# Kernel tuning notes

Hardware: AMD Instinct MI355X
Metric: run time of the kernel (lower is better)

## Reference

```python
import jax, jax.numpy as jnp
import numpy as np

U, I, D = 2048, 4096, 64


def setup_inputs() -> dict:
    key = jax.random.key(0)
    ks = jax.random.split(key, 16)
    s = 0.02  # weight scale (xavier-ish)
    inp = {
        "ui_input_mp": jax.random.uniform(ks[0], (U, I), jnp.float32),
        "ui_input_pmp": jax.random.uniform(ks[1], (U, I), jnp.float32),
        "Wu_mp": jax.random.normal(ks[2], (D, I), jnp.float32) * s,
        "Wu_pmp": jax.random.normal(ks[3], (D, I), jnp.float32) * s,
        "Wi_mp": jax.random.normal(ks[4], (D, U), jnp.float32) * s,
        "Wi_pmp": jax.random.normal(ks[5], (D, U), jnp.float32) * s,
        "mw_mp": jax.random.normal(ks[6], (I, D), jnp.float32) * s,
        "mb_mp": jnp.zeros((I,), jnp.float32),
        "aw_mp": jax.random.normal(ks[7], (I, I), jnp.float32) * s,
        "ab_mp": jnp.zeros((I,), jnp.float32),
        "Wat_mp": jax.random.normal(ks[8], (U, U + I), jnp.float32) * s,
        "mw_pmp": jax.random.normal(ks[9], (I, D), jnp.float32) * s,
        "mb_pmp": jnp.zeros((I,), jnp.float32),
        "aw_pmp": jax.random.normal(ks[10], (I, I), jnp.float32) * s,
        "ab_pmp": jnp.zeros((I,), jnp.float32),
        "Wat_pmp": jax.random.normal(ks[11], (U, U + I), jnp.float32) * s,
        "mlp_w": jax.random.normal(ks[12], (D, 2 * D), jnp.float32) * s,
        "mlp_b": jnp.zeros((D,), jnp.float32),
        "tr_w": jax.random.normal(ks[13], (D, D), jnp.float32) * s,
        "tr_b": jnp.zeros((D,), jnp.float32),
    }
    return inp


def _attention_weights(x, mw, mb, aw, ab, Wat):
    # x: [U+I, D]; mlp Linear(D,I)+ReLU (dropout=0), then tanh
    h = jnp.tanh(jax.nn.relu(x @ mw.T + mb))          # [U+I, I]
    a = jnp.tanh(h @ aw.T + ab)                        # [U+I, I]
    scores = Wat @ a                                   # [U, I]
    return jax.nn.softmax(scores, axis=1)


def _branch(ui, Wu, Wi, mw, mb, aw, ab, Wat):
    ue = ui @ Wu.T                                     # [U, D] user embeds
    ie = ui.T @ Wi.T                                   # [I, D] item embeds
    x = jnp.concatenate([ue, ie], axis=0)              # [U+I, D]
    at = _attention_weights(x, mw, mb, aw, ab, Wat)    # [U, I]
    ue_at = at @ ie                                    # [U, D]
    return ue, ie, ue_at


def reference(ui_input_mp, ui_input_pmp, Wu_mp, Wu_pmp, Wi_mp, Wi_pmp,
              mw_mp, mb_mp, aw_mp, ab_mp, Wat_mp,
              mw_pmp, mb_pmp, aw_pmp, ab_pmp, Wat_pmp,
              mlp_w, mlp_b, tr_w, tr_b):
    mlp = lambda z: jax.nn.sigmoid(z @ mlp_w.T + mlp_b)

    ue_mp, ie_mp, ue_mp_at = _branch(ui_input_mp, Wu_mp, Wi_mp,
                                     mw_mp, mb_mp, aw_mp, ab_mp, Wat_mp)
    ue_pmp, ie_pmp, ue_pmp_at = _branch(ui_input_pmp, Wu_pmp, Wi_pmp,
                                        mw_pmp, mb_pmp, aw_pmp, ab_pmp, Wat_pmp)

    u_mp = mlp(jnp.concatenate([ue_mp, ue_mp_at], axis=1))      # [U, D]
    u_pmp = mlp(jnp.concatenate([ue_pmp, ue_pmp_at], axis=1))   # [U, D]

    rate = jax.nn.sigmoid(u_mp + u_pmp)
    user_fusion = rate * u_mp + (1.0 - rate) * u_pmp            # [U, D]

    item_embeddings = mlp(jnp.concatenate([ie_mp, ie_pmp], axis=1))  # [I, D]

    user_embeds = jnp.tanh(user_fusion @ tr_w.T + tr_b)          # [U, D]
    return user_embeds, item_embeddings
```

## Files before the change

kernel.cpp:

```cpp
#include <hip/hip_runtime.h>
#include <stdint.h>
#include <math.h>


typedef short short8 __attribute__((ext_vector_type(8)));
typedef unsigned short ushort8 __attribute__((ext_vector_type(8)));
typedef unsigned char uchar8 __attribute__((ext_vector_type(8)));
typedef float f32x4 __attribute__((ext_vector_type(4)));
typedef int int4v __attribute__((ext_vector_type(4)));
typedef int int8v __attribute__((ext_vector_type(8)));

#define DEVI static __device__ __forceinline__

DEVI unsigned short f2bf(float f) {
  uint32_t u = __builtin_bit_cast(uint32_t, f);
  return (unsigned short)((u + 0x7fffu + ((u >> 16) & 1u)) >> 16);
}
DEVI unsigned char f2fp8(float f) {
  uint32_t u = __builtin_bit_cast(uint32_t, f);
  uint32_t s = (u >> 24) & 0x80u;
  uint32_t a = u & 0x7fffffffu;
  if (a >= 0x43e00000u) return (unsigned char)(s | 0x7eu);
  if (a < 0x3c800000u) {
    float af = __builtin_bit_cast(float, a);
    uint32_t n = (uint32_t)__builtin_rintf(af * 512.0f);
    return (unsigned char)(s | n);
  }
  uint32_t r = a + 0xfffffu + ((a >> 20) & 1u);
  return (unsigned char)(s | ((r >> 20) - 960u));
}
DEVI float sigmoidf_(float x) { return 1.0f / (1.0f + expf(-x)); }

DEVI void gld16(const void* g, void* l) {
  __builtin_amdgcn_global_load_lds(
      (const __attribute__((address_space(1))) unsigned int*)g,
      (__attribute__((address_space(3))) unsigned int*)l, 16, 0, 0);
}

#define MFMA16B(a, b, c) __builtin_amdgcn_mfma_f32_16x16x32_bf16(a, b, c, 0, 0, 0)
#define MFMAMX(a, b, c)                                              \
  __builtin_amdgcn_mfma_scale_f32_16x16x128_f8f6f4(                  \
      a, b, c, 0, 0, 0, 0x7f7f7f7fu, 0, 0x7f7f7f7fu)

__global__ __launch_bounds__(256) void k_f32_to_bf16(
    const float* __restrict__ s, unsigned short* __restrict__ d, long n) {
  long i0 = ((long)blockIdx.x * 256 + threadIdx.x) * 8;
  long stride = (long)gridDim.x * 256 * 8;
  for (long i = i0; i < n; i += stride) {
    f32x4 a = *(const f32x4*)(s + i);
    f32x4 b = *(const f32x4*)(s + i + 4);
    ushort8 o;
    o[0] = f2bf(a[0]); o[1] = f2bf(a[1]); o[2] = f2bf(a[2]); o[3] = f2bf(a[3]);
    o[4] = f2bf(b[0]); o[5] = f2bf(b[1]); o[6] = f2bf(b[2]); o[7] = f2bf(b[3]);
    *(ushort8*)(d + i) = o;
  }
}

__global__ __launch_bounds__(256) void k_f32_to_fp8(
    const float* __restrict__ s, unsigned char* __restrict__ d, long n,
    float scale) {
  long i0 = ((long)blockIdx.x * 256 + threadIdx.x) * 8;
  long stride = (long)gridDim.x * 256 * 8;
  for (long i = i0; i < n; i += stride) {
    f32x4 a = *(const f32x4*)(s + i);
    f32x4 b = *(const f32x4*)(s + i + 4);
    uchar8 o;
    o[0] = f2fp8(a[0] * scale); o[1] = f2fp8(a[1] * scale);
    o[2] = f2fp8(a[2] * scale); o[3] = f2fp8(a[3] * scale);
    o[4] = f2fp8(b[0] * scale); o[5] = f2fp8(b[1] * scale);
    o[6] = f2fp8(b[2] * scale); o[7] = f2fp8(b[3] * scale);
    *(uchar8*)(d + i) = o;
  }
}

template <int EPI>
__global__ __launch_bounds__(256) void k_gemmMX(
    const unsigned char* __restrict__ A0, const unsigned char* __restrict__ A1,
    const unsigned char* __restrict__ B0, const unsigned char* __restrict__ B1,
    float* __restrict__ outF, unsigned char* __restrict__ oB0,
    unsigned char* __restrict__ oB1, const float* __restrict__ bias0,
    const float* __restrict__ bias1, int M, int N, int K, long zsf,
    float dsc) {
  const int gx = gridDim.x;
  const int nwg = gx * gridDim.y;
  const int flat = blockIdx.y * gx + blockIdx.x;
  const int swz = (flat & 7) * (nwg >> 3) + (flat >> 3);
  const int bxi = swz % gx, byi = swz / gx;

  const int bz = blockIdx.z;
  const unsigned char* A = bz ? A1 : A0;
  const unsigned char* B = bz ? B1 : B0;
  unsigned char* outB = bz ? oB1 : oB0;
  const float* bias = bz ? bias1 : bias0;

  __shared__ unsigned char lds[2][2][16384];
  const int tid = threadIdx.x, lane = tid & 63;
  const int wid = tid >> 6, wr = wid >> 1, wc = wid & 1;
  const int bm = bxi * 128, bn = byi * 128;
  const int rl = lane & 15, q = lane >> 4;

  const int x7 = rl & 7;
  const int c0 = ((2 * q) ^ x7) << 4;
  const int c1 = ((2 * q + 1) ^ x7) << 4;

  size_t soff[4];
  int dsto[4];
#pragma unroll
  for (int i = 0; i < 4; i++) {
    const int cid = tid + 256 * i;
    const int r = cid >> 3, c = cid & 7;
    soff[i] = (size_t)r * K + ((c ^ (r & 7)) << 4);
    dsto[i] = cid << 4;
  }

  const unsigned char* gA = A + (size_t)bm * K;
  const unsigned char* gB = B + (size_t)bn * K;

  auto stage = [&](int k0, int buf) {
#pragma unroll
    for (int i = 0; i < 4; i++) {
      gld16(gA + k0 + soff[i], &lds[buf][0][dsto[i]]);
      gld16(gB + k0 + soff[i], &lds[buf][1][dsto[i]]);
    }
  };

  f32x4 acc[4][4] = {};

  stage(0, 0);
  asm volatile("s_waitcnt vmcnt(0)\ns_barrier" ::: "memory");

  int buf = 0;
  for (int k0 = 0; k0 < K; k0 += 128) {
    if (k0 + 128 < K) stage(k0 + 128, buf ^ 1);

    const unsigned char* As = &lds[buf][0][0];
    const unsigned char* Bs = &lds[buf][1][0];
    int8v af[4], bf[4];
#pragma unroll
    for (int mi = 0; mi < 4; mi++) {
      const unsigned char* p = As + (wr * 64 + mi * 16 + rl) * 128;
      int4v lo = *(const int4v*)(p + c0);
      int4v hi = *(const int4v*)(p + c1);
      af[mi] = __builtin_shufflevector(lo, hi, 0, 1, 2, 3, 4, 5, 6, 7);
    }
#pragma unroll
    for (int ni = 0; ni < 4; ni++) {
      const unsigned char* p = Bs + (wc * 64 + ni * 16 + rl) * 128;
      int4v lo = *(const int4v*)(p + c0);
      int4v hi = *(const int4v*)(p + c1);
      bf[ni] = __builtin_shufflevector(lo, hi, 0, 1, 2, 3, 4, 5, 6, 7);
    }

    __builtin_amdgcn_s_setprio(1);
#pragma unroll
    for (int mi = 0; mi < 4; mi++)
#pragma unroll
      for (int ni = 0; ni < 4; ni++)
        acc[mi][ni] = MFMAMX(af[mi], bf[ni], acc[mi][ni]);
    __builtin_amdgcn_s_setprio(0);

    if (k0 + 128 < K) {
      asm volatile("s_waitcnt vmcnt(0)\ns_barrier" ::: "memory");
      buf ^= 1;
    }
  }

#pragma unroll
  for (int mi = 0; mi < 4; mi++) {
#pragma unroll
    for (int ni = 0; ni < 4; ni++) {
      const int col = bn + wc * 64 + ni * 16 + rl;
#pragma unroll
      for (int r = 0; r < 4; r++) {
        const int row = bm + wr * 64 + mi * 16 + q * 4 + r;
        const float v = acc[mi][ni][r] * dsc;
        if (EPI == 0)
          outF[(long)bz * zsf + (size_t)row * N + col] = v;
        else
          outB[(size_t)row * N + col] = f2fp8(tanhf(v + bias[row]));
      }
    }
  }
}

__global__ __launch_bounds__(256) void k_gemmH(
    const unsigned short* __restrict__ A0, const unsigned short* __restrict__ A1,
    const unsigned short* __restrict__ B0, const unsigned short* __restrict__ B1,
    unsigned char* __restrict__ o0, unsigned char* __restrict__ o1,
    const float* __restrict__ bias0, const float* __restrict__ bias1, int M,
    int N, int K) {
  const int bz = blockIdx.z;
  const unsigned short* A = bz ? A1 : A0;
  const unsigned short* B = bz ? B1 : B0;
  unsigned char* out8 = bz ? o1 : o0;
  const float* bias = bz ? bias1 : bias0;

  __shared__ unsigned short As[128 * 32];
  __shared__ unsigned short Bs[128 * 32];
  const int tid = threadIdx.x, lane = tid & 63, wid = tid >> 6;
  const int wr = wid >> 1, wc = wid & 1;
  const int bm = blockIdx.x * 128, bn = blockIdx.y * 128;
  const int c0 = tid, c1 = tid + 256;
  const int s0 = ((c0 & 3) ^ ((c0 >> 3) & 3)) << 3;
  const int s1 = ((c1 & 3) ^ ((c1 >> 3) & 3)) << 3;
  const int rl = lane & 15, q = lane >> 4;
  const int qe = (q ^ ((rl >> 1) & 3)) << 3;

  f32x4 acc[4][4] = {};

  for (int k0 = 0; k0 < K; k0 += 32) {
    gld16(A + (size_t)(bm + (c0 >> 2)) * K + k0 + s0, As + c0 * 8);
    gld16(A + (size_t)(bm + (c1 >> 2)) * K + k0 + s1, As + c1 * 8);
    gld16(B + (size_t)(bn + (c0 >> 2)) * K + k0 + s0, Bs + c0 * 8);
    gld16(B + (size_t)(bn + (c1 >> 2)) * K + k0 + s1, Bs + c1 * 8);
    __syncthreads();

    short8 af[4], bfr[4];
#pragma unroll
    for (int mi = 0; mi < 4; mi++)
      af[mi] = *(const short8*)(As + (wr * 64 + mi * 16 + rl) * 32 + qe);
#pragma unroll
    for (int ni = 0; ni < 4; ni++)
      bfr[ni] = *(const short8*)(Bs + (wc * 64 + ni * 16 + rl) * 32 + qe);
#pragma unroll
    for (int mi = 0; mi < 4; mi++)
#pragma unroll
      for (int ni = 0; ni < 4; ni++)
        acc[mi][ni] = MFMA16B(af[mi], bfr[ni], acc[mi][ni]);
    __syncthreads();
  }

#pragma unroll
  for (int mi = 0; mi < 4; mi++) {
#pragma unroll
    for (int ni = 0; ni < 4; ni++) {
      const int col = bn + wc * 64 + ni * 16 + rl;
#pragma unroll
      for (int r = 0; r < 4; r++) {
        const int row = bm + wr * 64 + mi * 16 + q * 4 + r;
        out8[(size_t)row * N + col] =
            f2fp8(tanhf(fmaxf(acc[mi][ni][r] + bias[col], 0.0f)));
      }
    }
  }
}

template <int AMODE, int BMODE>
__global__ __launch_bounds__(256) void k_sgemm64s(
    const void* __restrict__ A0, const void* __restrict__ A1,
    const void* __restrict__ B0, const void* __restrict__ B1,
    float* __restrict__ P, int kchunk, int lda, int ldb, int M) {
  const int br = blockIdx.z, kz = blockIdx.y, KS = gridDim.y;
  const void* Av = br ? A1 : A0;
  const void* Bv = br ? B1 : B0;

  __shared__ unsigned short As[64 * 40];
  __shared__ unsigned short Bs[64 * 40];
  const int tid = threadIdx.x, lane = tid & 63, w = tid >> 6;
  const int tm = blockIdx.x * 64;

  f32x4 acc[4] = {};
  const int kbeg = kz * kchunk, kend = kbeg + kchunk;

  for (int k0 = kbeg; k0 < kend; k0 += 32) {
    if (AMODE == 0) {
      const float* Af = (const float*)Av;
      const int m = tid >> 2, k8 = (tid & 3) << 3;
      f32x4 x0 = *(const f32x4*)(Af + (size_t)(tm + m) * lda + k0 + k8);
      f32x4 x1 = *(const f32x4*)(Af + (size_t)(tm + m) * lda + k0 + k8 + 4);
      ushort8 o;
      o[0] = f2bf(x0[0]); o[1] = f2bf(x0[1]); o[2] = f2bf(x0[2]); o[3] = f2bf(x0[3]);
      o[4] = f2bf(x1[0]); o[5] = f2bf(x1[1]); o[6] = f2bf(x1[2]); o[7] = f2bf(x1[3]);
      *(ushort8*)(As + m * 40 + k8) = o;
    } else if (AMODE == 1) {
      const float* Af = (const float*)Av;
#pragma unroll
      for (int t = 0; t < 2; t++) {
        const int c = tid + t * 256;
        const int u = c >> 4, i4 = (c & 15) << 2;
        f32x4 x = *(const f32x4*)(Af + (size_t)(k0 + u) * lda + tm + i4);
        As[(i4 + 0) * 40 + u] = f2bf(x[0]);
        As[(i4 + 1) * 40 + u] = f2bf(x[1]);
        As[(i4 + 2) * 40 + u] = f2bf(x[2]);
        As[(i4 + 3) * 40 + u] = f2bf(x[3]);
      }
    } else {
      const unsigned short* Ab = (const unsigned short*)Av;
      const int m = tid >> 2, k8 = (tid & 3) << 3;
      *(ushort8*)(As + m * 40 + k8) =
          *(const ushort8*)(Ab + (size_t)(tm + m) * lda + k0 + k8);
    }
    if (BMODE == 0) {
      const float* Bf = (const float*)Bv;
      const int n = tid >> 2, k8 = (tid & 3) << 3;
      f32x4 x0 = *(const f32x4*)(Bf + (size_t)n * ldb + k0 + k8);
      f32x4 x1 = *(const f32x4*)(Bf + (size_t)n * ldb + k0 + k8 + 4);
      ushort8 o;
      o[0] = f2bf(x0[0]); o[1] = f2bf(x0[1]); o[2] = f2bf(x0[2]); o[3] = f2bf(x0[3]);
      o[4] = f2bf(x1[0]); o[5] = f2bf(x1[1]); o[6] = f2bf(x1[2]); o[7] = f2bf(x1[3]);
      *(ushort8*)(Bs + n * 40 + k8) = o;
    } else {
      const unsigned short* Bb = (const unsigned short*)Bv;
      const int n = tid >> 2, k8 = (tid & 3) << 3;
      *(ushort8*)(Bs + n * 40 + k8) =
          *(const ushort8*)(Bb + (size_t)n * ldb + k0 + k8);
    }
    __syncthreads();

    const int kr = (lane >> 4) << 3;
    short8 a = *(const short8*)(As + (w * 16 + (lane & 15)) * 40 + kr);
#pragma unroll
    for (int ni = 0; ni < 4; ni++) {
      short8 bb = *(const short8*)(Bs + (ni * 16 + (lane & 15)) * 40 + kr);
      acc[ni] = MFMA16B(a, bb, acc[ni]);
    }
    __syncthreads();
  }

  float* out = P + ((size_t)(br * KS + kz) * M) * 64;
#pragma unroll
  for (int ni = 0; ni < 4; ni++) {
    const int col = ni * 16 + (lane & 15);
#pragma unroll
    for (int r = 0; r < 4; r++) {
      const int row = tm + w * 16 + ((lane >> 4) << 2) + r;
      out[(size_t)row * 64 + col] = acc[ni][r];
    }
  }
}

template <int WF, int WB, int WT>
__global__ __launch_bounds__(256) void k_reduce(
    const float* __restrict__ P, size_t pbr_stride, float* F0, float* F1,
    unsigned short* Bo0, unsigned short* Bo1, unsigned short* T0,
    unsigned short* T1, int M, int KS, int ldT) {
  const int br = blockIdx.y;
  const float* Pp = P + (size_t)br * pbr_stride;
  const size_t i = (size_t)blockIdx.x * 256 + threadIdx.x;
  const size_t n = (size_t)M * 64;
  float s = 0.f;
  for (int k = 0; k < KS; k++) s += Pp[(size_t)k * n + i];
  if (WF) (br ? F1 : F0)[i] = s;
  if (WB) (br ? Bo1 : Bo0)[i] = f2bf(s);
  if (WT) {
    const int row = (int)(i >> 6), col = (int)(i & 63);
    (br ? T1 : T0)[(size_t)col * ldT + row] = f2bf(s);
  }
}

__global__ __launch_bounds__(256) void k_softmax(
    const float* __restrict__ S, unsigned short* __restrict__ P0,
    unsigned short* __restrict__ P1, long slab) {
  const int row = blockIdx.x, br = blockIdx.y, tid = threadIdx.x;
  const float* s = S + (size_t)br * slab + (size_t)row * 4096;
  float v[16];
  float m = -1e30f;
#pragma unroll
  for (int j = 0; j < 16; j++) {
    v[j] = s[tid + j * 256];
    m = fmaxf(m, v[j]);
  }
  __shared__ float red[4], red2[4];
  for (int o = 32; o; o >>= 1) m = fmaxf(m, __shfl_down(m, o));
  if ((tid & 63) == 0) red[tid >> 6] = m;
  __syncthreads();
  m = fmaxf(fmaxf(red[0], red[1]), fmaxf(red[2], red[3]));
  float sum = 0.0f;
#pragma unroll
  for (int j = 0; j < 16; j++) {
    v[j] = expf(v[j] - m);
    sum += v[j];
  }
  for (int o = 32; o; o >>= 1) sum += __shfl_down(sum, o);
  if ((tid & 63) == 0) red2[tid >> 6] = sum;
  __syncthreads();
  const float inv = 1.0f / (red2[0] + red2[1] + red2[2] + red2[3]);
  unsigned short* p = (br ? P1 : P0) + (size_t)row * 4096;
#pragma unroll
  for (int j = 0; j < 16; j++) p[tid + j * 256] = f2bf(v[j] * inv);
}

__global__ __launch_bounds__(256) void k_user(
    const float* __restrict__ ue_mp, const float* __restrict__ ueat_mp,
    const float* __restrict__ ue_pmp, const float* __restrict__ ueat_pmp,
    const float* __restrict__ mlp_w, const float* __restrict__ mlp_b,
    const float* __restrict__ tr_w, const float* __restrict__ tr_b,
    float* __restrict__ out) {
  const int tid = threadIdx.x, d = tid & 63, w = tid >> 6;
  const int m = blockIdx.x * 4 + w;
  __shared__ float fus[4][64];
  float a1 = mlp_b[d], a2 = a1;
  const float* r1 = ue_mp + (size_t)m * 64;
  const float* r2 = ueat_mp + (size_t)m * 64;
  const float* r3 = ue_pmp + (size_t)m * 64;
  const float* r4 = ueat_pmp + (size_t)m * 64;
  const float* w1 = mlp_w + (size_t)d * 128;
#pragma unroll 8
  for (int k = 0; k < 64; k++) {
    const float wv = w1[k];
    a1 += r1[k] * wv;
    a2 += r3[k] * wv;
  }
#pragma unroll 8
  for (int k = 0; k < 64; k++) {
    const float wv = w1[64 + k];
    a1 += r2[k] * wv;
    a2 += r4[k] * wv;
  }
  const float u1 = sigmoidf_(a1), u2 = sigmoidf_(a2);
  const float rate = sigmoidf_(u1 + u2);
  fus[w][d] = rate * u1 + (1.0f - rate) * u2;
  __syncthreads();
  float o = tr_b[d];
  const float* tw = tr_w + (size_t)d * 64;
#pragma unroll 8
  for (int k = 0; k < 64; k++) o += fus[w][k] * tw[k];
  out[(size_t)m * 64 + d] = tanhf(o);
}

__global__ __launch_bounds__(256) void k_item(
    const float* __restrict__ ie_mp, const float* __restrict__ ie_pmp,
    const float* __restrict__ mlp_w, const float* __restrict__ mlp_b,
    float* __restrict__ out) {
  const int tid = threadIdx.x, d = tid & 63, w = tid >> 6;
  const int i = blockIdx.x * 4 + w;
  float a = mlp_b[d];
  const float* r1 = ie_mp + (size_t)i * 64;
  const float* r2 = ie_pmp + (size_t)i * 64;
  const float* wp = mlp_w + (size_t)d * 128;
#pragma unroll 8
  for (int k = 0; k < 64; k++) {
    a += r1[k] * wp[k];
    a += r2[k] * wp[64 + k];
  }
  out[(size_t)i * 64 + d] = sigmoidf_(a);
}

extern "C" void kernel_launch(void* const* d_in, const int* in_sizes, int n_in,
                              void* d_out, int out_size, void* d_ws,
                              size_t ws_size, hipStream_t stream) {
  const int U = 2048, I = 4096, D = 64, UI = 6144;
  const float WSC = 16.0f, DSC = 1.0f / 16.0f;

  const float* ui[2] = {(const float*)d_in[0], (const float*)d_in[1]};
  const float* Wu[2] = {(const float*)d_in[2], (const float*)d_in[3]};
  const float* Wi[2] = {(const float*)d_in[4], (const float*)d_in[5]};
  const float* mw[2] = {(const float*)d_in[6], (const float*)d_in[11]};
  const float* mb[2] = {(const float*)d_in[7], (const float*)d_in[12]};
  const float* aw[2] = {(const float*)d_in[8], (const float*)d_in[13]};
  const float* ab[2] = {(const float*)d_in[9], (const float*)d_in[14]};
  const float* Wat[2] = {(const float*)d_in[10], (const float*)d_in[15]};
  const float* mlp_w = (const float*)d_in[16];
  const float* mlp_b = (const float*)d_in[17];
  const float* tr_w = (const float*)d_in[18];
  const float* tr_b = (const float*)d_in[19];

  char* ws = (char*)d_ws;
  size_t off = 0;
  auto alloc = [&](size_t bytes) {
    void* p = ws + off;
    off += (bytes + 255) & ~(size_t)255;
    return p;
  };
  unsigned char* aw_f8[2] = {(unsigned char*)alloc((size_t)I * I),
                             (unsigned char*)alloc((size_t)I * I)};
  unsigned short* mw_bf[2] = {(unsigned short*)alloc((size_t)I * D * 2),
                              (unsigned short*)alloc((size_t)I * D * 2)};
  unsigned char* h_f8[2] = {(unsigned char*)alloc((size_t)UI * I),
                            (unsigned char*)alloc((size_t)UI * I)};
  unsigned char* aT_f8[2] = {(unsigned char*)alloc((size_t)I * UI),
                             (unsigned char*)alloc((size_t)I * UI)};
  float* scores = (float*)alloc((size_t)U * I * 4 * 2);
  unsigned short* at_bf[2] = {(unsigned short*)alloc((size_t)U * I * 2),
                              (unsigned short*)alloc((size_t)U * I * 2)};
  unsigned short* x_bf[2];
  float* ue_f[2];
  float* ie_f[2];
  unsigned short* ieT[2];
  float* ueat_f[2];
  for (int b = 0; b < 2; b++) {
    x_bf[b] = (unsigned short*)alloc((size_t)UI * D * 2);
    ue_f[b] = (float*)alloc((size_t)U * D * 4);
    ie_f[b] = (float*)alloc((size_t)I * D * 4);
    ieT[b] = (unsigned short*)alloc((size_t)D * I * 2);
    ueat_f[b] = (float*)alloc((size_t)U * D * 4);
  }
  float* pue = (float*)h_f8[0];
  float* pie = (float*)aT_f8[0];
  float* pueat = scores;
  unsigned char* Wat_f8[2] = {(unsigned char*)at_bf[0],
                              (unsigned char*)at_bf[1]};
  const long zsf = (long)U * I;

  const dim3 blk(256);

  k_sgemm64s<0, 0><<<dim3(U / 64, 8, 2), blk, 0, stream>>>(
      ui[0], ui[1], Wu[0], Wu[1], pue, I / 8, I, I, U);
  k_reduce<1, 1, 0><<<dim3(U * 64 / 256, 2), blk, 0, stream>>>(
      pue, (size_t)8 * U * 64, ue_f[0], ue_f[1], x_bf[0], x_bf[1], nullptr,
      nullptr, U, 8, 0);
  k_sgemm64s<1, 0><<<dim3(I / 64, 8, 2), blk, 0, stream>>>(
      ui[0], ui[1], Wi[0], Wi[1], pie, U / 8, I, U, I);
  k_reduce<1, 1, 1><<<dim3(I * 64 / 256, 2), blk, 0, stream>>>(
      pie, (size_t)8 * I * 64, ie_f[0], ie_f[1], x_bf[0] + (size_t)U * D,
      x_bf[1] + (size_t)U * D, ieT[0], ieT[1], I, 8, I);

  for (int b = 0; b < 2; b++) {
    k_f32_to_fp8<<<2048, blk, 0, stream>>>(aw[b], aw_f8[b], (long)I * I, WSC);
    k_f32_to_fp8<<<2048, blk, 0, stream>>>(Wat[b], Wat_f8[b], (long)U * UI, WSC);
    k_f32_to_bf16<<<128, blk, 0, stream>>>(mw[b], mw_bf[b], (long)I * D);
  }

  k_gemmH<<<dim3(UI / 128, I / 128, 2), blk, 0, stream>>>(
      x_bf[0], x_bf[1], mw_bf[0], mw_bf[1], h_f8[0], h_f8[1], mb[0], mb[1],
      UI, I, D);

  k_gemmMX<1><<<dim3(I / 128, UI / 128, 2), blk, 0, stream>>>(
      aw_f8[0], aw_f8[1], h_f8[0], h_f8[1], nullptr, aT_f8[0], aT_f8[1],
      ab[0], ab[1], I, UI, I, 0, DSC);

  k_gemmMX<0><<<dim3(U / 128, I / 128, 2), blk, 0, stream>>>(
      Wat_f8[0], Wat_f8[1], aT_f8[0], aT_f8[1], scores, nullptr, nullptr,
      nullptr, nullptr, U, I, UI, zsf, DSC);

  k_softmax<<<dim3(U, 2), blk, 0, stream>>>(scores, at_bf[0], at_bf[1], zsf);

  k_sgemm64s<2, 2><<<dim3(U / 64, 8, 2), blk, 0, stream>>>(
      at_bf[0], at_bf[1], ieT[0], ieT[1], pueat, I / 8, I, I, U);
  k_reduce<1, 0, 0><<<dim3(U * 64 / 256, 2), blk, 0, stream>>>(
      pueat, (size_t)8 * U * 64, ueat_f[0], ueat_f[1], nullptr, nullptr,
      nullptr, nullptr, U, 8, 0);

  float* out_user = (float*)d_out;
  float* out_item = (float*)d_out + (size_t)U * D;
  k_user<<<U / 4, blk, 0, stream>>>(ue_f[0], ueat_f[0], ue_f[1], ueat_f[1],
                                    mlp_w, mlp_b, tr_w, tr_b, out_user);
  k_item<<<I / 4, blk, 0, stream>>>(ie_f[0], ie_f[1], mlp_w, mlp_b, out_item);
}
```

Measured before the change: 639.7 us.

## Enlarge MX fp8 GEMM tiles to 256x256 with 512-thread workgroups

The fp8 MX GEMM kernel now computes 256x256 output tiles per workgroup using 8 waves (2x4), with each wave owning 128x64 and a 8x4 accumulator array. LDS staging doubles to 64KB per double buffer, and the K loop is manually unrolled by two to alternate buffers statically. A-fragments are loaded in two halves to limit register pressure. The aim is higher arithmetic intensity and fewer global/LDS loads per MFMA, at the cost of fewer workgroups (e.g. 8x16x2 for the scores GEMM), more registers, and occupancy capped at one block per CU.

```diff
diff --git a/kernel.cpp b/kernel.cpp
--- a/kernel.cpp
+++ b/kernel.cpp
@@ -74,7 +74,7 @@
 }
 
 template <int EPI>
-__global__ __launch_bounds__(256) void k_gemmMX(
+__global__ __launch_bounds__(512, 1) void k_gemmMX(
     const unsigned char* __restrict__ A0, const unsigned char* __restrict__ A1,
     const unsigned char* __restrict__ B0, const unsigned char* __restrict__ B1,
     float* __restrict__ outF, unsigned char* __restrict__ oB0,
@@ -93,10 +93,10 @@
   unsigned char* outB = bz ? oB1 : oB0;
   const float* bias = bz ? bias1 : bias0;
 
-  __shared__ unsigned char lds[2][2][16384];
+  __shared__ unsigned char lds[2][2][32768];
   const int tid = threadIdx.x, lane = tid & 63;
-  const int wid = tid >> 6, wr = wid >> 1, wc = wid & 1;
-  const int bm = bxi * 128, bn = byi * 128;
+  const int wid = tid >> 6, wr = wid >> 2, wc = wid & 3;
+  const int bm = bxi * 256, bn = byi * 256;
   const int rl = lane & 15, q = lane >> 4;
 
   const int x7 = rl & 7;
@@ -107,7 +107,7 @@
   int dsto[4];
 #pragma unroll
   for (int i = 0; i < 4; i++) {
-    const int cid = tid + 256 * i;
+    const int cid = tid + 512 * i;
     const int r = cid >> 3, c = cid & 7;
     soff[i] = (size_t)r * K + ((c ^ (r & 7)) << 4);
     dsto[i] = cid << 4;
@@ -116,64 +116,82 @@
   const unsigned char* gA = A + (size_t)bm * K;
   const unsigned char* gB = B + (size_t)bn * K;
 
-  auto stage = [&](int k0, int buf) {
+  auto stage = [&](int kc, int buf) {
 #pragma unroll
     for (int i = 0; i < 4; i++) {
-      gld16(gA + k0 + soff[i], &lds[buf][0][dsto[i]]);
-      gld16(gB + k0 + soff[i], &lds[buf][1][dsto[i]]);
+      gld16(gA + kc + soff[i], &lds[buf][0][dsto[i]]);
+      gld16(gB + kc + soff[i], &lds[buf][1][dsto[i]]);
     }
   };
 
-  f32x4 acc[4][4] = {};
-
-  stage(0, 0);
-  asm volatile("s_waitcnt vmcnt(0)\ns_barrier" ::: "memory");
-
-  int buf = 0;
-  for (int k0 = 0; k0 < K; k0 += 128) {
-    if (k0 + 128 < K) stage(k0 + 128, buf ^ 1);
-
-    const unsigned char* As = &lds[buf][0][0];
-    const unsigned char* Bs = &lds[buf][1][0];
-    int8v af[4], bf[4];
+  f32x4 acc[8][4] = {};
+
+  auto body = [&](int kc, int bc, int bn_) {
+    if (kc + 128 < K) stage(kc + 128, bn_);
+
+    const unsigned char* As = &lds[bc][0][0];
+    const unsigned char* Bs = &lds[bc][1][0];
+
+    int8v bf[4];
+#pragma unroll
+    for (int nf = 0; nf < 4; nf++) {
+      const unsigned char* p = Bs + (wc * 64 + nf * 16 + rl) * 128;
+      int4v lo = *(const int4v*)(p + c0);
+      int4v hi = *(const int4v*)(p + c1);
+      bf[nf] = __builtin_shufflevector(lo, hi, 0, 1, 2, 3, 4, 5, 6, 7);
+    }
+    int8v af[4];
 #pragma unroll
     for (int mi = 0; mi < 4; mi++) {
-      const unsigned char* p = As + (wr * 64 + mi * 16 + rl) * 128;
+      const unsigned char* p = As + (wr * 128 + mi * 16 + rl) * 128;
       int4v lo = *(const int4v*)(p + c0);
       int4v hi = *(const int4v*)(p + c1);
       af[mi] = __builtin_shufflevector(lo, hi, 0, 1, 2, 3, 4, 5, 6, 7);
     }
-#pragma unroll
-    for (int ni = 0; ni < 4; ni++) {
-      const unsigned char* p = Bs + (wc * 64 + ni * 16 + rl) * 128;
+    __builtin_amdgcn_s_setprio(1);
+#pragma unroll
+    for (int mi = 0; mi < 4; mi++)
+#pragma unroll
+      for (int nf = 0; nf < 4; nf++)
+        acc[mi][nf] = MFMAMX(af[mi], bf[nf], acc[mi][nf]);
+    __builtin_amdgcn_s_setprio(0);
+#pragma unroll
+    for (int mi = 0; mi < 4; mi++) {
+      const unsigned char* p = As + (wr * 128 + (4 + mi) * 16 + rl) * 128;
       int4v lo = *(const int4v*)(p + c0);
       int4v hi = *(const int4v*)(p + c1);
-      bf[ni] = __builtin_shufflevector(lo, hi, 0, 1, 2, 3, 4, 5, 6, 7);
-    }
-
+      af[mi] = __builtin_shufflevector(lo, hi, 0, 1, 2, 3, 4, 5, 6, 7);
+    }
     __builtin_amdgcn_s_setprio(1);
 #pragma unroll
     for (int mi = 0; mi < 4; mi++)
 #pragma unroll
-      for (int ni = 0; ni < 4; ni++)
-        acc[mi][ni] = MFMAMX(af[mi], bf[ni], acc[mi][ni]);
+      for (int nf = 0; nf < 4; nf++)
+        acc[4 + mi][nf] = MFMAMX(af[mi], bf[nf], acc[4 + mi][nf]);
     __builtin_amdgcn_s_setprio(0);
 
-    if (k0 + 128 < K) {
+    if (kc + 128 < K) {
       asm volatile("s_waitcnt vmcnt(0)\ns_barrier" ::: "memory");
-      buf ^= 1;
-    }
-  }
-
-#pragma unroll
-  for (int mi = 0; mi < 4; mi++) {
-#pragma unroll
-    for (int ni = 0; ni < 4; ni++) {
-      const int col = bn + wc * 64 + ni * 16 + rl;
+    }
+  };
+
+  stage(0, 0);
+  asm volatile("s_waitcnt vmcnt(0)\ns_barrier" ::: "memory");
+
+  for (int k0 = 0; k0 < K; k0 += 256) {
+    body(k0, 0, 1);
+    body(k0 + 128, 1, 0);
+  }
+
+#pragma unroll
+  for (int m = 0; m < 8; m++) {
+#pragma unroll
+    for (int nf = 0; nf < 4; nf++) {
+      const int col = bn + wc * 64 + nf * 16 + rl;
 #pragma unroll
       for (int r = 0; r < 4; r++) {
-        const int row = bm + wr * 64 + mi * 16 + q * 4 + r;
-        const float v = acc[mi][ni][r] * dsc;
+        const int row = bm + wr * 128 + m * 16 + q * 4 + r;
+        const float v = acc[m][nf][r] * dsc;
         if (EPI == 0)
           outF[(long)bz * zsf + (size_t)row * N + col] = v;
         else
@@ -515,11 +533,11 @@
       x_bf[0], x_bf[1], mw_bf[0], mw_bf[1], h_f8[0], h_f8[1], mb[0], mb[1],
       UI, I, D);
 
-  k_gemmMX<1><<<dim3(I / 128, UI / 128, 2), blk, 0, stream>>>(
+  k_gemmMX<1><<<dim3(I / 256, UI / 256, 2), dim3(512), 0, stream>>>(
       aw_f8[0], aw_f8[1], h_f8[0], h_f8[1], nullptr, aT_f8[0], aT_f8[1],
       ab[0], ab[1], I, UI, I, 0, DSC);
 
-  k_gemmMX<0><<<dim3(U / 128, I / 128, 2), blk, 0, stream>>>(
+  k_gemmMX<0><<<dim3(U / 256, I / 256, 2), dim3(512), 0, stream>>>(
       Wat_f8[0], Wat_f8[1], aT_f8[0], aT_f8[1], scores, nullptr, nullptr,
       nullptr, nullptr, U, I, UI, zsf, DSC);
 
```

Result: slower. 735.8 us (+15.0%).
